# Kernel optimization log

Hardware: AMD Instinct MI355X
Metric: run time of the kernel (lower is better)

The kernel has to match this reference:

```python
import jax, jax.numpy as jnp
import numpy as np

N = 50000
E = 800000
HIGH, LOW, EMB = 128, 32, 64
HID, HEADS, OUT = 32, 8, 8
IN1 = HIGH + EMB  # 192
IN2 = HID * HEADS  # 256
NEG_SLOPE = 0.2


def setup_inputs() -> dict:
    key = jax.random.key(0)
    ks = jax.random.split(key, 12)
    s = lambda k, shape: (jax.random.normal(k, shape, dtype=jnp.float32) * 0.1)
    return {
        "high_dim_features": jax.random.normal(ks[0], (N, HIGH), dtype=jnp.float32),
        "low_dim_features": jax.random.normal(ks[1], (N, LOW), dtype=jnp.float32),
        "edge_index": jax.random.randint(ks[2], (2, E), 0, N, dtype=jnp.int32),
        "W_emb": s(ks[3], (LOW, EMB)),
        "b_emb": jnp.zeros((EMB,), jnp.float32),
        "W1": s(ks[4], (IN1, HEADS * HID)),
        "att_src1": s(ks[5], (HEADS, HID)),
        "att_dst1": s(ks[6], (HEADS, HID)),
        "b1": jnp.zeros((HEADS * HID,), jnp.float32),
        "W2": s(ks[7], (IN2, OUT)),
        "att_src2": s(ks[8], (1, OUT)),
        "att_dst2": s(ks[9], (1, OUT)),
        "b2": jnp.zeros((OUT,), jnp.float32),
    }


def _gat_layer(x, src, dst, W, att_src, att_dst, bias, heads, out_ch, concat):
    # x: [N, F_in]; src/dst: [E'] (self-loops already appended)
    n = x.shape[0]
    h = (x @ W).reshape(n, heads, out_ch)            # [N, H, C]
    a_src = jnp.einsum('nhc,hc->nh', h, att_src)     # [N, H]
    a_dst = jnp.einsum('nhc,hc->nh', h, att_dst)
    alpha = a_src[src] + a_dst[dst]                  # [E', H]
    alpha = jax.nn.leaky_relu(alpha, NEG_SLOPE)
    # segment softmax over incoming edges per destination node
    m = jax.ops.segment_max(alpha, dst, num_segments=n)
    ea = jnp.exp(alpha - m[dst])
    z = jax.ops.segment_sum(ea, dst, num_segments=n)
    alpha = ea / (z[dst] + 1e-16)                    # [E', H]
    msg = h[src] * alpha[:, :, None]                 # [E', H, C]
    out = jax.ops.segment_sum(msg, dst, num_segments=n)  # [N, H, C]
    if concat:
        out = out.reshape(n, heads * out_ch)
    else:
        out = out.mean(axis=1)
    return out + bias


def reference(high_dim_features, low_dim_features, edge_index,
              W_emb, b_emb, W1, att_src1, att_dst1, b1,
              W2, att_src2, att_dst2, b2):
    # embedding + elu, concat
    emb = jax.nn.elu(low_dim_features @ W_emb + b_emb)
    x = jnp.concatenate([high_dim_features, emb], axis=1)  # [N, IN1]
    # add self-loops (PyG default)
    loops = jnp.arange(N, dtype=edge_index.dtype)
    src = jnp.concatenate([edge_index[0], loops])
    dst = jnp.concatenate([edge_index[1], loops])
    x = _gat_layer(x, src, dst, W1, att_src1, att_dst1, b1, HEADS, HID, True)
    x = jax.nn.elu(x)  # dropout: eval mode no-op
    x = _gat_layer(x, src, dst, W2, att_src2, att_dst2, b2, 1, OUT, False)
    return jax.nn.log_softmax(x, axis=1)
```

## Files before the change

kernel.cpp:

```cpp
#include <hip/hip_runtime.h>
#include <hip/hip_bf16.h>

typedef __hip_bfloat16 bf16;
typedef short bf16x8 __attribute__((ext_vector_type(8)));
typedef float f32x4  __attribute__((ext_vector_type(4)));

#define CHK 2048

__device__ __forceinline__ float bf2f(bf16 v){ return __bfloat162float(v); }
__device__ __forceinline__ bf16  f2bf(float f){ return __float2bfloat16(f); }
__device__ __forceinline__ float lrelu(float a){ return a > 0.f ? a : 0.2f*a; }
__device__ __forceinline__ float bfbits(short s){
    union{unsigned u; float f;} cv; cv.u = ((unsigned)(unsigned short)s) << 16; return cv.f;
}
__device__ __forceinline__ short bf16s(float f){ bf16 q = f2bf(f); return *(short*)&q; }
__device__ __forceinline__ float cvtf(const void* p, int i, int isb){
    return isb ? bf2f(((const bf16*)p)[i]) : ((const float*)p)[i];
}
__device__ __forceinline__ short cvts(const void* p, int i, int isb){
    return isb ? ((const short*)p)[i] : bf16s(((const float*)p)[i]);
}
__device__ __forceinline__ bf16x8 load8(const void* base, size_t off, int isb){
    if (isb) return *(const bf16x8*)((const bf16*)base + off);
    const float* f = (const float*)base + off;
    f32x4 v0 = *(const f32x4*)f;
    f32x4 v1 = *(const f32x4*)(f + 4);
    short r[8];
    #pragma unroll
    for (int j = 0; j < 4; j++) r[j]   = bf16s(v0[j]);
    #pragma unroll
    for (int j = 0; j < 4; j++) r[4+j] = bf16s(v1[j]);
    return *(const bf16x8*)r;
}

__global__ __launch_bounds__(256) void k_init(const unsigned short* __restrict__ raw,
        int* __restrict__ flag, const int* __restrict__ dst,
        int* __restrict__ bucketCnt, int E, int NBUK, int nBlk){
    __shared__ int h[256];
    int t = threadIdx.x;
    if (blockIdx.x == 0){
        unsigned short w = raw[2*t];
        int e = (w >> 7) & 0xFF;
        int ok = (e >= 90 && e <= 140) ? 1 : 0;
        __shared__ int cnt;
        if (t == 0) cnt = 0;
        __syncthreads();
        atomicAdd(&cnt, ok);
        __syncthreads();
        if (t == 0) *flag = (cnt >= 192) ? 1 : 0;
    }
    h[t] = 0;
    __syncthreads();
    for (int i = blockIdx.x*256 + t; i < E; i += nBlk*256)
        atomicAdd(&h[((unsigned)dst[i]) >> 8], 1);
    __syncthreads();
    if (t < NBUK && h[t]) atomicAdd(&bucketCnt[t], h[t]);
}

__global__ __launch_bounds__(256) void k_prep(const void* __restrict__ low,
        const void* __restrict__ Wemb, const void* __restrict__ bemb,
        const void* __restrict__ W1, const void* __restrict__ W2,
        bf16* __restrict__ emb, bf16* __restrict__ Bp, bf16* __restrict__ Bp2,
        const int* __restrict__ flag, int N, int nEmb){
    __shared__ float wem[2048 + 64];
    __shared__ short lows[1024];
    int t = threadIdx.x;
    int b = blockIdx.x;
    int isb = *flag;
    if (b >= nEmb){
        int i = (b - nEmb)*256 + t;
        if (i < 16*6*64*8){
            int j = i & 7;
            int lane = (i >> 3) & 63;
            int r = i >> 9;
            int kt = r % 6, nt = r / 6;
            int k = kt*32 + (lane >> 4)*8 + j;
            int n = nt*16 + (lane & 15);
            *(short*)&Bp[i] = cvts(W1, k*256 + n, isb);
        } else {
            int i2 = i - 16*6*64*8;
            if (i2 >= 8*64*8) return;
            int j = i2 & 7;
            int lane = (i2 >> 3) & 63;
            int kt = i2 >> 9;
            int k = kt*32 + (lane >> 4)*8 + j;
            int n = lane & 15;
            *(short*)&Bp2[i2] = (n < 8) ? cvts(W2, k*8 + n, isb) : (short)0;
        }
        return;
    }
    for (int i = t; i < 2048; i += 256) wem[i] = cvtf(Wemb, i, isb);
    if (t < 64) wem[2048 + t] = cvtf(bemb, t, isb);
    int nl = t >> 3, j8 = (t & 7) * 8;
    for (int tile = 0; tile < 4; tile++){
        int nb0 = b*128 + tile*32;
        __syncthreads();
        int lim = (N - nb0) * 32;
        if (lim > 1024) lim = 1024;
        if (lim < 0) lim = 0;
        for (int i = t; i < 1024; i += 256)
            lows[i] = (i < lim) ? cvts(low, nb0*32 + i, isb) : (short)0;
        __syncthreads();
        float acc[8];
        #pragma unroll
        for (int j = 0; j < 8; j++) acc[j] = wem[2048 + j8 + j];
        for (int k = 0; k < 32; k++){
            float lv = bfbits(lows[nl*32 + k]);
            f32x4 w0 = *(const f32x4*)&wem[k*64 + j8];
            f32x4 w1 = *(const f32x4*)&wem[k*64 + j8 + 4];
            #pragma unroll
            for (int j = 0; j < 4; j++) acc[j]   += lv * w0[j];
            #pragma unroll
            for (int j = 0; j < 4; j++) acc[4+j] += lv * w1[j];
        }
        int n = nb0 + nl;
        if (n < N){
            short ov[8];
            #pragma unroll
            for (int j = 0; j < 8; j++){
                float v = acc[j];
                ov[j] = bf16s(v > 0.f ? v : expm1f(v));
            }
            *(bf16x8*)&emb[(size_t)n*64 + j8] = *(const bf16x8*)ov;
        }
    }
}

__global__ __launch_bounds__(256) void k_bscan(const int* __restrict__ bucketCnt,
        int* __restrict__ bucketPtr, int* __restrict__ bucketCur,
        int* __restrict__ rowptr, int N, int E, int NBUK){
    __shared__ int sd[256];
    int t = threadIdx.x;
    int v = (t < NBUK) ? bucketCnt[t] : 0;
    sd[t] = v;
    __syncthreads();
    #pragma unroll
    for (int off = 1; off < 256; off <<= 1){
        int a = (t >= off) ? sd[t - off] : 0;
        __syncthreads();
        sd[t] += a;
        __syncthreads();
    }
    int excl = sd[t] - v;
    if (t < NBUK){ bucketPtr[t] = excl; bucketCur[t*16] = excl; }
    if (t == 0){ bucketPtr[NBUK] = sd[255]; rowptr[N] = E + N; }
}

__global__ __launch_bounds__(256, 3) void k_sg(
        const int* __restrict__ ei, int* __restrict__ bucketCur, int* __restrict__ pk,
        const void* __restrict__ highv, const bf16* __restrict__ emb,
        const bf16* __restrict__ Bp, const void* __restrict__ attS,
        const void* __restrict__ attD, bf16* __restrict__ h1,
        float* __restrict__ a_s, float* __restrict__ a_d,
        const int* __restrict__ flag, int N, int E, int nScat, int NBUK){
    const int RS = 260;
    __shared__ union SM {
        struct { float eb[16*260 + 16]; float att[512]; } g;
        struct { unsigned short dstS[CHK]; int hist[4][256]; int cur[4][256]; } s;
    } sm;
    int t = threadIdx.x;
    if ((int)blockIdx.x < nScat){
        int base = blockIdx.x * CHK;
        int cnt = E - base; if (cnt > CHK) cnt = CHK;
        int wv = t >> 6, lane = t & 63;
        #pragma unroll
        for (int w = 0; w < 4; w++) sm.s.hist[w][t] = 0;
        __syncthreads();
        const int* dstp = ei + E + base;
        const int* srcp = ei + base;
        int per = (cnt + 3) >> 2;
        int wb = wv*per, we = wb + per;
        if (we > cnt) we = cnt;
        if (wb > cnt) wb = cnt;
        for (int i = wb + lane; i < we; i += 64){
            int d = dstp[i];
            sm.s.dstS[i] = (unsigned short)d;
            atomicAdd(&sm.s.hist[wv][((unsigned)d) >> 8], 1);
        }
        __syncthreads();
        if (t < NBUK){
            int h0 = sm.s.hist[0][t], h1v = sm.s.hist[1][t];
            int h2 = sm.s.hist[2][t], h3 = sm.s.hist[3][t];
            int c = h0 + h1v + h2 + h3;
            int bs = c ? atomicAdd(&bucketCur[t*16], c) : 0;
            sm.s.cur[0][t] = bs;
            sm.s.cur[1][t] = bs + h0;
            sm.s.cur[2][t] = bs + h0 + h1v;
            sm.s.cur[3][t] = bs + h0 + h1v + h2;
        }
        __syncthreads();
        for (int i = wb + lane; i < we; i += 64){
            int d = sm.s.dstS[i];
            int pos = atomicAdd(&sm.s.cur[wv][d >> 8], 1);
            pk[pos] = ((d & 255) << 24) | srcp[i];
        }
        return;
    }
    float* eb  = sm.g.eb;
    float* att = sm.g.att;
    int isb = *flag;
    att[t] = cvtf(attS, t, isb);
    att[256 + t] = cvtf(attD, t, isb);
    int w = t >> 6, lane = t & 63;
    int m_lo = lane & 15, quad = lane >> 4;
    int m0 = (blockIdx.x - nScat) * 64;
    int mr[4];
    #pragma unroll
    for (int rt = 0; rt < 4; rt++){
        int m = m0 + rt*16 + m_lo;
        mr[rt] = m < N ? m : N-1;
    }
    f32x4 acc[4][4];
    #pragma unroll
    for (int rt = 0; rt < 4; rt++)
        #pragma unroll
        for (int ct = 0; ct < 4; ct++) acc[rt][ct] = (f32x4){0.f,0.f,0.f,0.f};

    #pragma unroll 2
    for (int kt = 0; kt < 6; kt++){
        bf16x8 a[4], b[4];
        if (kt < 4){
            #pragma unroll
            for (int rt = 0; rt < 4; rt++)
                a[rt] = load8(highv, (size_t)mr[rt]*128 + kt*32 + quad*8, isb);
        } else {
            #pragma unroll
            for (int rt = 0; rt < 4; rt++)
                a[rt] = *(const bf16x8*)&emb[(size_t)mr[rt]*64 + (kt-4)*32 + quad*8];
        }
        #pragma unroll
        for (int ct = 0; ct < 4; ct++)
            b[ct] = *(const bf16x8*)&Bp[(size_t)(((w*4 + ct)*6 + kt)*64 + lane)*8];
        #pragma unroll
        for (int rt = 0; rt < 4; rt++)
            #pragma unroll
            for (int ct = 0; ct < 4; ct++)
                acc[rt][ct] = __builtin_amdgcn_mfma_f32_16x16x32_bf16(a[rt], b[ct], acc[rt][ct], 0, 0, 0);
    }

    #pragma unroll 1
    for (int rt = 0; rt < 4; rt++){
        __syncthreads();
        #pragma unroll
        for (int ct = 0; ct < 4; ct++)
            #pragma unroll
            for (int reg = 0; reg < 4; reg++)
                eb[(quad*4 + reg)*RS + w*64 + ct*16 + m_lo] = acc[rt][ct][reg];
        __syncthreads();
        int r = t >> 4, cb = t & 15;
        int c0 = cb * 16;
        int m = m0 + rt*16 + r;
        f32x4 v[4];
        #pragma unroll
        for (int p = 0; p < 4; p++) v[p] = *(const f32x4*)&eb[r*RS + c0 + p*4];
        float ps = 0.f, pd = 0.f;
        #pragma unroll
        for (int p = 0; p < 4; p++)
            #pragma unroll
            for (int j = 0; j < 4; j++){
                ps += v[p][j] * att[c0 + p*4 + j];
                pd += v[p][j] * att[256 + c0 + p*4 + j];
            }
        if (m < N){
            short ov[16];
            #pragma unroll
            for (int p = 0; p < 4; p++)
                #pragma unroll
                for (int j = 0; j < 4; j++) ov[p*4+j] = bf16s(v[p][j]);
            *(bf16x8*)&h1[(size_t)m*256 + c0]     = *(const bf16x8*)&ov[0];
            *(bf16x8*)&h1[(size_t)m*256 + c0 + 8] = *(const bf16x8*)&ov[8];
        }
        ps += __shfl_xor(ps, 1);
        pd += __shfl_xor(pd, 1);
        if (((t & 1) == 0) && m < N){
            int hd = cb >> 1;
            a_s[m*8 + hd] = ps;
            a_d[m*8 + hd] = pd;
        }
    }
}

__global__ __launch_bounds__(256) void k_fine(const int* __restrict__ bucketPtr,
        const int* __restrict__ pk, int* __restrict__ rowptr, int* __restrict__ srcs,
        int N){
    __shared__ int hist[4][256];
    __shared__ int cur[4][256];
    __shared__ int sd[256];
    int t = threadIdx.x;
    int wv = t >> 6, lane = t & 63;
    int b = blockIdx.x;
    int d0 = b << 8;
    int nd = N - d0; if (nd > 256) nd = 256; if (nd < 0) nd = 0;
    int ebeg = bucketPtr[b], eend = bucketPtr[b+1];
    int tot = eend - ebeg;
    int per = (tot + 3) >> 2;
    int wb = wv*per, we = wb + per;
    if (we > tot) we = tot;
    if (wb > tot) wb = tot;
    #pragma unroll
    for (int w = 0; w < 4; w++) hist[w][t] = 0;
    __syncthreads();
    for (int i = wb + lane; i < we; i += 64)
        atomicAdd(&hist[wv][((unsigned)pk[ebeg + i]) >> 24], 1);
    __syncthreads();
    int h0 = hist[0][t], h1 = hist[1][t], h2 = hist[2][t], h3 = hist[3][t];
    int selfc = (t < nd) ? 1 : 0;
    int v = selfc + h0 + h1 + h2 + h3;
    sd[t] = v;
    __syncthreads();
    #pragma unroll
    for (int off = 1; off < 256; off <<= 1){
        int a = (t >= off) ? sd[t - off] : 0;
        __syncthreads();
        sd[t] += a;
        __syncthreads();
    }
    int r = ebeg + d0 + sd[t] - v;
    if (t < nd){
        rowptr[d0 + t] = r;
        srcs[r] = d0 + t;
    }
    int c0 = r + selfc;
    cur[0][t] = c0;
    cur[1][t] = c0 + h0;
    cur[2][t] = c0 + h0 + h1;
    cur[3][t] = c0 + h0 + h1 + h2;
    __syncthreads();
    for (int i = wb + lane; i < we; i += 64){
        int p = pk[ebeg + i];
        int pos = atomicAdd(&cur[wv][((unsigned)p) >> 24], 1);
        srcs[pos] = p & 0xFFFFFF;
    }
}

__global__ __launch_bounds__(256) void k_edge1(const int* __restrict__ rowptr,
        const int* __restrict__ srcs, const float* __restrict__ a_s,
        const float* __restrict__ a_d, const bf16* __restrict__ h1,
        const void* __restrict__ b1, bf16* __restrict__ x2,
        const int* __restrict__ flag, int N){
    int t = threadIdx.x;
    int lane = t & 63, wv = t >> 6;
    int n = blockIdx.x*4 + wv;
    if (n >= N) return;
    int beg = rowptr[n];
    int deg = rowptr[n+1] - beg;

    int cl = lane & 31;
    int hb = cl >> 2;
    int half = lane >> 5;
    float adb = a_d[n*8 + hb];

    float acc[8];
    #pragma unroll
    for (int j = 0; j < 8; j++) acc[j] = 0.f;
    float z = 0.f;

    int e = half;
    for (; e + 6 < deg; e += 8){
        int s0 = srcs[beg + e];
        int s1 = srcs[beg + e + 2];
        int s2 = srcs[beg + e + 4];
        int s3 = srcs[beg + e + 6];
        float w0 = __expf(fminf(lrelu(a_s[s0*8 + hb] + adb), 80.f));
        float w1 = __expf(fminf(lrelu(a_s[s1*8 + hb] + adb), 80.f));
        float w2 = __expf(fminf(lrelu(a_s[s2*8 + hb] + adb), 80.f));
        float w3 = __expf(fminf(lrelu(a_s[s3*8 + hb] + adb), 80.f));
        bf16x8 v0 = *(const bf16x8*)&h1[(size_t)s0*256 + cl*8];
        bf16x8 v1 = *(const bf16x8*)&h1[(size_t)s1*256 + cl*8];
        bf16x8 v2 = *(const bf16x8*)&h1[(size_t)s2*256 + cl*8];
        bf16x8 v3 = *(const bf16x8*)&h1[(size_t)s3*256 + cl*8];
        z += (w0 + w1) + (w2 + w3);
        #pragma unroll
        for (int j = 0; j < 8; j++) acc[j] += w0 * bfbits(v0[j]);
        #pragma unroll
        for (int j = 0; j < 8; j++) acc[j] += w1 * bfbits(v1[j]);
        #pragma unroll
        for (int j = 0; j < 8; j++) acc[j] += w2 * bfbits(v2[j]);
        #pragma unroll
        for (int j = 0; j < 8; j++) acc[j] += w3 * bfbits(v3[j]);
    }
    for (; e < deg; e += 2){
        int s = srcs[beg + e];
        float w = __expf(fminf(lrelu(a_s[s*8 + hb] + adb), 80.f));
        bf16x8 hv = *(const bf16x8*)&h1[(size_t)s*256 + cl*8];
        z += w;
        #pragma unroll
        for (int j = 0; j < 8; j++) acc[j] += w * bfbits(hv[j]);
    }
    #pragma unroll
    for (int j = 0; j < 8; j++) acc[j] += __shfl_xor(acc[j], 32);
    z += __shfl_xor(z, 32);
    float rz = 1.f / (z + 1e-16f);

    if (half == 0){
        int isb = *flag;
        bf16x8 bv = load8(b1, cl*8, isb);
        short ov[8];
        #pragma unroll
        for (int j = 0; j < 8; j++){
            float v = acc[j] * rz + bfbits(bv[j]);
            ov[j] = bf16s(v > 0.f ? v : expm1f(v));
        }
        *(bf16x8*)&x2[(size_t)n*256 + cl*8] = *(const bf16x8*)ov;
    }
}

__global__ __launch_bounds__(256) void k_gemm2(const bf16* __restrict__ x2,
        const bf16* __restrict__ Bp2, const void* __restrict__ attS,
        const void* __restrict__ attD, float* __restrict__ h2,
        float* __restrict__ a2s, float* __restrict__ a2d,
        const int* __restrict__ flag, int N){
    int t = threadIdx.x;
    int isb = *flag;
    int w = t >> 6, lane = t & 63;
    int m_lo = lane & 15, quad = lane >> 4;
    int m0 = blockIdx.x*64 + w*16;
    int mr = m0 + m_lo; if (mr >= N) mr = N-1;
    f32x4 acc = (f32x4){0.f,0.f,0.f,0.f};
    #pragma unroll
    for (int kt = 0; kt < 8; kt++){
        bf16x8 a = *(const bf16x8*)&x2[(size_t)mr*256 + kt*32 + quad*8];
        bf16x8 b = *(const bf16x8*)&Bp2[(size_t)(kt*64 + lane)*8];
        acc = __builtin_amdgcn_mfma_f32_16x16x32_bf16(a, b, acc, 0, 0, 0);
    }
    float s2 = (m_lo < 8) ? cvtf(attS, m_lo, isb) : 0.f;
    float d2 = (m_lo < 8) ? cvtf(attD, m_lo, isb) : 0.f;
    #pragma unroll
    for (int reg = 0; reg < 4; reg++){
        int m = m0 + quad*4 + reg;
        float val = acc[reg];
        float ps = val * s2, pd = val * d2;
        ps += __shfl_xor(ps, 1); ps += __shfl_xor(ps, 2);
        ps += __shfl_xor(ps, 4); ps += __shfl_xor(ps, 8);
        pd += __shfl_xor(pd, 1); pd += __shfl_xor(pd, 2);
        pd += __shfl_xor(pd, 4); pd += __shfl_xor(pd, 8);
        if (m < N){
            if (m_lo < 8) h2[(size_t)m*8 + m_lo] = val;
            if (m_lo == 0){ a2s[m] = ps; a2d[m] = pd; }
        }
    }
}

__global__ __launch_bounds__(256) void k_edge2(const int* __restrict__ rowptr,
        const int* __restrict__ srcs, const float* __restrict__ a2s,
        const float* __restrict__ a2d, const float* __restrict__ h2,
        const void* __restrict__ b2, void* __restrict__ outv,
        const int* __restrict__ flag, int N){
    int t = threadIdx.x;
    int lane = t & 63, wv = t >> 6;
    int n = blockIdx.x*4 + wv;
    if (n >= N) return;
    int beg = rowptr[n];
    int deg = rowptr[n+1] - beg;
    float adh = a2d[n];
    int ep = lane >> 3, c = lane & 7;
    float acc = 0.f, z = 0.f;
    for (int e = ep; e < deg; e += 8){
        int s = srcs[beg + e];
        float w = __expf(fminf(lrelu(a2s[s] + adh), 80.f));
        z += w;
        acc += w * h2[(size_t)s*8 + c];
    }
    acc += __shfl_xor(acc, 8);
    acc += __shfl_xor(acc, 16);
    acc += __shfl_xor(acc, 32);
    z += __shfl_xor(z, 8);
    z += __shfl_xor(z, 16);
    z += __shfl_xor(z, 32);
    int isb = *flag;
    float val = acc / (z + 1e-16f) + cvtf(b2, c, isb);
    float mx = val;
    mx = fmaxf(mx, __shfl_xor(mx, 1));
    mx = fmaxf(mx, __shfl_xor(mx, 2));
    mx = fmaxf(mx, __shfl_xor(mx, 4));
    float se = __expf(val - mx);
    se += __shfl_xor(se, 1); se += __shfl_xor(se, 2); se += __shfl_xor(se, 4);
    float r = val - mx - __logf(se);
    if (lane < 8){
        if (isb) ((bf16*)outv)[(size_t)n*8 + c] = f2bf(r);
        else     ((float*)outv)[(size_t)n*8 + c] = r;
    }
}

extern "C" void kernel_launch(void* const* d_in, const int* in_sizes, int n_in,
                              void* d_out, int out_size, void* d_ws, size_t ws_size,
                              hipStream_t stream) {
    const int* ei = (const int*)d_in[2];
    const int N = in_sizes[0] / 128;
    const int E = in_sizes[2] / 2;
    const int ET = E + N;
    const int NBUK = (N + 255) >> 8;

    char* p = (char*)d_ws;
    auto alloc = [&](size_t bytes) -> void* {
        char* r = p;
        p += (bytes + 255) & ~(size_t)255;
        return (void*)r;
    };
    int*   flag      = (int*)  alloc(256);
    int*   bucketCnt = (int*)  alloc((size_t)NBUK*4);
    int*   bucketPtr = (int*)  alloc((size_t)(NBUK+1)*4);
    int*   bucketCur = (int*)  alloc((size_t)NBUK*16*4);
    int*   rowptr    = (int*)  alloc((size_t)(N+1)*4);
    int*   srcs      = (int*)  alloc((size_t)ET*4);
    int*   pk        = (int*)  alloc((size_t)E*4);
    bf16*  Bp        = (bf16*) alloc((size_t)192*256*2);
    bf16*  Bp2       = (bf16*) alloc((size_t)8*64*8*2);
    bf16*  emb       = (bf16*) alloc((size_t)N*64*2);
    bf16*  h1        = (bf16*) alloc((size_t)N*256*2);
    float* a_s       = (float*)alloc((size_t)N*8*4);
    float* a_d       = (float*)alloc((size_t)N*8*4);
    bf16*  x2        = (bf16*) alloc((size_t)N*256*2);
    float* h2        = (float*)alloc((size_t)N*8*4);
    float* a2s       = (float*)alloc((size_t)N*4);
    float* a2d       = (float*)alloc((size_t)N*4);

    hipMemsetAsync(bucketCnt, 0, (size_t)NBUK*4, stream);
    k_init<<<256, 256, 0, stream>>>((const unsigned short*)d_in[0], flag,
            ei + E, bucketCnt, E, NBUK, 256);
    {
        int nEmb  = (N + 127)/128;
        int nPack = (16*6*64*8 + 8*64*8 + 255)/256;
        k_prep<<<nEmb + nPack, 256, 0, stream>>>(d_in[1], d_in[3], d_in[4],
                d_in[5], d_in[9], emb, Bp, Bp2, flag, N, nEmb);
    }
    k_bscan<<<1, 256, 0, stream>>>(bucketCnt, bucketPtr, bucketCur, rowptr, N, E, NBUK);
    {
        int nG = (N + 63)/64;
        int nScat = (E + CHK - 1)/CHK;
        k_sg<<<nScat + nG, 256, 0, stream>>>(ei, bucketCur, pk,
                d_in[0], emb, Bp, d_in[6], d_in[7], h1, a_s, a_d, flag, N, E, nScat, NBUK);
    }
    k_fine<<<NBUK, 256, 0, stream>>>(bucketPtr, pk, rowptr, srcs, N);
    k_edge1<<<(N + 3)/4, 256, 0, stream>>>(rowptr, srcs, a_s, a_d, h1, d_in[8], x2, flag, N);
    k_gemm2<<<(N + 63)/64, 256, 0, stream>>>(x2, Bp2, d_in[10], d_in[11], h2, a2s, a2d, flag, N);
    k_edge2<<<(N + 3)/4, 256, 0, stream>>>(rowptr, srcs, a2s, a2d, h2, d_in[12], d_out, flag, N);
}
```

Baseline: 315.6 us.

## Stage A tile of first GAT GEMM in XOR-swizzled shared memory

The 64-row A tile (high-dim features and embedding) is now loaded cooperatively into LDS with an XOR swizzle, and the MFMA loop reads A from shared memory. Before, each of the four waves loaded the same rows straight from global memory. The change removes that four-way redundant global traffic and gives coalesced 16-byte loads. In exchange it uses more LDS (about 24KB for A) and drops the occupancy hint of 3 blocks per CU from launch bounds, so occupancy may fall.

```diff
diff --git a/kernel.cpp b/kernel.cpp
--- a/kernel.cpp
+++ b/kernel.cpp
@@ -146,7 +146,7 @@
     if (t == 0){ bucketPtr[NBUK] = sd[255]; rowptr[N] = E + N; }
 }
 
-__global__ __launch_bounds__(256, 3) void k_sg(
+__global__ __launch_bounds__(256) void k_sg(
         const int* __restrict__ ei, int* __restrict__ bucketCur, int* __restrict__ pk,
         const void* __restrict__ highv, const bf16* __restrict__ emb,
         const bf16* __restrict__ Bp, const void* __restrict__ attS,
@@ -155,9 +155,11 @@
         const int* __restrict__ flag, int N, int E, int nScat, int NBUK){
     const int RS = 260;
     __shared__ union SM {
-        struct { float eb[16*260 + 16]; float att[512]; } g;
+        struct { short Ah[64*128]; short Ae[64*64]; } a;
+        struct { float eb[16*260 + 16]; } g;
         struct { unsigned short dstS[CHK]; int hist[4][256]; int cur[4][256]; } s;
     } sm;
+    __shared__ float att[512];
     int t = threadIdx.x;
     if ((int)blockIdx.x < nScat){
         int base = blockIdx.x * CHK;
@@ -196,37 +198,51 @@
         }
         return;
     }
-    float* eb  = sm.g.eb;
-    float* att = sm.g.att;
     int isb = *flag;
     att[t] = cvtf(attS, t, isb);
     att[256 + t] = cvtf(attD, t, isb);
     int w = t >> 6, lane = t & 63;
     int m_lo = lane & 15, quad = lane >> 4;
     int m0 = (blockIdx.x - nScat) * 64;
-    int mr[4];
-    #pragma unroll
-    for (int rt = 0; rt < 4; rt++){
-        int m = m0 + rt*16 + m_lo;
-        mr[rt] = m < N ? m : N-1;
-    }
+
+    #pragma unroll
+    for (int ii = 0; ii < 4; ii++){
+        int id = t + ii*256;
+        int r = id >> 4, c = id & 15;
+        int gr = m0 + r; if (gr >= N) gr = N-1;
+        bf16x8 v = load8(highv, (size_t)gr*128 + c*8, isb);
+        *(bf16x8*)&sm.a.Ah[r*128 + ((c ^ (r & 7)) << 3)] = v;
+    }
+    #pragma unroll
+    for (int ii = 0; ii < 2; ii++){
+        int id = t + ii*256;
+        int r = id >> 3, c = id & 7;
+        int gr = m0 + r; if (gr >= N) gr = N-1;
+        bf16x8 v = *(const bf16x8*)&emb[(size_t)gr*64 + c*8];
+        *(bf16x8*)&sm.a.Ae[r*64 + ((c ^ (r & 7)) << 3)] = v;
+    }
+    __syncthreads();
+
     f32x4 acc[4][4];
     #pragma unroll
     for (int rt = 0; rt < 4; rt++)
         #pragma unroll
         for (int ct = 0; ct < 4; ct++) acc[rt][ct] = (f32x4){0.f,0.f,0.f,0.f};
 
+    int sw = m_lo & 7;
     #pragma unroll 2
     for (int kt = 0; kt < 6; kt++){
         bf16x8 a[4], b[4];
         if (kt < 4){
+            int ch = (kt*4 + quad) ^ sw;
             #pragma unroll
             for (int rt = 0; rt < 4; rt++)
-                a[rt] = load8(highv, (size_t)mr[rt]*128 + kt*32 + quad*8, isb);
+                a[rt] = *(const bf16x8*)&sm.a.Ah[(rt*16 + m_lo)*128 + (ch << 3)];
         } else {
+            int ch = ((kt-4)*4 + quad) ^ sw;
             #pragma unroll
             for (int rt = 0; rt < 4; rt++)
-                a[rt] = *(const bf16x8*)&emb[(size_t)mr[rt]*64 + (kt-4)*32 + quad*8];
+                a[rt] = *(const bf16x8*)&sm.a.Ae[(rt*16 + m_lo)*64 + (ch << 3)];
         }
         #pragma unroll
         for (int ct = 0; ct < 4; ct++)
@@ -238,6 +254,7 @@
                 acc[rt][ct] = __builtin_amdgcn_mfma_f32_16x16x32_bf16(a[rt], b[ct], acc[rt][ct], 0, 0, 0);
     }
 
+    float* eb = sm.g.eb;
     #pragma unroll 1
     for (int rt = 0; rt < 4; rt++){
         __syncthreads();
```

Result: faster. 303.0 us (-4.0%).
